# Performance work log

Hardware: AMD Instinct MI355X
Metric: run time of the kernel (lower is better)

Reference implementation:

```python
import jax, jax.numpy as jnp
import numpy as np

B, N, D = 256, 100000, 512
A, C, K = 256, 100, 32
EPS = 1e-8  # torch cosine_similarity eps


def setup_inputs() -> dict:
    key = jax.random.key(0)
    ks = jax.random.split(key, 10)
    s = lambda fan_in: 1.0 / np.sqrt(fan_in)
    return {
        "query_feat": jax.random.normal(ks[0], (B, D), jnp.float32),
        "memory_keys": jax.random.normal(ks[1], (N, D), jnp.float32),
        # query_dense: Linear(D, A)
        "Wq": jax.random.uniform(ks[2], (D, A), jnp.float32, -s(D), s(D)),
        "bq": jax.random.uniform(ks[3], (A,), jnp.float32, -s(D), s(D)),
        # memory_dense: Linear(D, A)
        "Wm": jax.random.uniform(ks[4], (D, A), jnp.float32, -s(D), s(D)),
        "bm": jax.random.uniform(ks[5], (A,), jnp.float32, -s(D), s(D)),
        # attention_score_dense: Linear(A, 1)
        "Ws": jax.random.uniform(ks[6], (A, 1), jnp.float32, -s(A), s(A)),
        "bs": jax.random.uniform(ks[7], (1,), jnp.float32, -s(A), s(A)),
        # classification_layer: Linear(2*D, C)
        "Wc": jax.random.uniform(ks[8], (2 * D, C), jnp.float32, -s(2 * D), s(2 * D)),
        "bc": jax.random.uniform(ks[9], (C,), jnp.float32, -s(2 * D), s(2 * D)),
    }


def reference(query_feat, memory_keys, Wq, bq, Wm, bm, Ws, bs, Wc, bc):
    # query embedding (visual encoder output) + relu
    q = jax.nn.relu(query_feat)  # [B, D]
    # ---- knn_search: cosine similarity + topk + gather ----
    qn = jnp.linalg.norm(q, axis=-1)            # [B]
    kn = jnp.linalg.norm(memory_keys, axis=-1)  # [N]
    sim = (q @ memory_keys.T) / jnp.maximum(qn[:, None] * kn[None, :], EPS)  # [B, N]
    _, idx = jax.lax.top_k(sim, K)              # [B, K]
    knn = memory_keys[idx]                      # [B, K, D]
    # ---- MemoryAttentionModule ----
    # tanh(query_dense(q)[:,None,:] + memory_dense(knn)) -> score -> softmax over K
    h = jnp.tanh((q @ Wq + bq)[:, None, :] + knn @ Wm + bm)  # [B, K, A]
    scores = h @ Ws + bs                                      # [B, K, 1]
    w = jax.nn.softmax(scores, axis=1)                        # [B, K, 1]
    attended = jnp.sum(w * knn, axis=1)                       # [B, D]
    # ---- classification ----
    merged = jnp.concatenate([q, attended], axis=1)           # [B, 2D]
    return merged @ Wc + bc                                   # [B, C]
```

## Files before the change

### kernel.cpp

```cpp
#include <hip/hip_runtime.h>
#include <hip/hip_bf16.h>
#include <hip/hip_fp16.h>

#define BQ    256
#define NKEY  100000
#define DD    512
#define AD    256
#define CD    100
#define KSEL  32
#define KB    64
#define NB    1563
#define CPQ   (NB*12)

#define NPART 8
#define WTOP  12
#define NC2   (NPART*4*WTOP)
#define TLA   6

typedef __attribute__((ext_vector_type(8))) short  short8_t;
typedef __attribute__((ext_vector_type(8))) __bf16 bf16x8;
typedef __attribute__((ext_vector_type(4))) float  f32x4;

__device__ __forceinline__ unsigned short f2bf(float x) {
  unsigned int u = __float_as_uint(x);
  return (unsigned short)((u + 0x7FFFu + ((u >> 16) & 1u)) >> 16);
}
__device__ __forceinline__ unsigned short f2bf_n(float x) {
  __bf16 h = (__bf16)x;
  return __builtin_bit_cast(unsigned short, h);
}
__device__ __forceinline__ float bf2f(unsigned short h) {
  return __uint_as_float(((unsigned int)h) << 16);
}
__device__ __forceinline__ f32x4 mfma_bf16(short8_t a, short8_t b, f32x4 c) {
  return __builtin_amdgcn_mfma_f32_16x16x32_bf16(
      __builtin_bit_cast(bf16x8, a), __builtin_bit_cast(bf16x8, b), c, 0, 0, 0);
}
__device__ __forceinline__ float fast_tanh(float x) {
  x = fminf(fmaxf(x, -15.f), 15.f);
  float e = __expf(2.f * x);
  return (e - 1.f) * __builtin_amdgcn_rcpf(e + 1.f);
}

template<int T>
__device__ __forceinline__ void topk_insert(float (&v)[T], int (&ix)[T], float val, int idx) {
  if (val <= v[T-1]) return;
  v[T-1] = val; ix[T-1] = idx;
  #pragma unroll
  for (int j = T-1; j > 0; --j) {
    bool sw = v[j] > v[j-1];
    float tv = sw ? v[j] : v[j-1];  float uv = sw ? v[j-1] : v[j];
    int   ti = sw ? ix[j] : ix[j-1]; int  ui = sw ? ix[j-1] : ix[j];
    v[j-1] = tv; v[j] = uv; ix[j-1] = ti; ix[j] = ui;
  }
}

__global__ __launch_bounds__(256) void k0_prep(const float* __restrict__ qfeat,
                                               const float* __restrict__ Wm,
                                               float* __restrict__ qr,
                                               unsigned short* __restrict__ qf,
                                               float* __restrict__ qn,
                                               unsigned short* __restrict__ wmf) {
  int b = blockIdx.x, t = threadIdx.x;
  if (b >= BQ) {
    int i = (b - BQ)*256 + t;
    int d = i >> 8, a = i & 255;
    wmf[(((a>>4)*64 + (d>>3))*16 + (a&15))*8 + (d&7)] = f2bf(Wm[i]);
    return;
  }
  float s = 0.f;
  #pragma unroll
  for (int p = 0; p < 2; ++p) {
    int k = t + p*256;
    float v = qfeat[b*DD + k];
    v = v > 0.f ? v : 0.f;
    qr[b*DD + k] = v;
    qf[(((b>>4)*64 + (k>>3))*16 + (b&15))*8 + (k&7)] = f2bf(v);
    s += v*v;
  }
  __shared__ float red[4];
  #pragma unroll
  for (int st = 1; st < 64; st <<= 1) s += __shfl_xor(s, st, 64);
  if ((t & 63) == 0) red[t>>6] = s;
  __syncthreads();
  if (t == 0) qn[b] = sqrtf(red[0]+red[1]+red[2]+red[3]);
}

__global__ __launch_bounds__(256) void k_qq(const float* __restrict__ Wq,
                                            const unsigned short* __restrict__ qf,
                                            const float* __restrict__ bq,
                                            const float* __restrict__ bm,
                                            float* __restrict__ qq) {
  __shared__ unsigned short wb[64*16*8];
  int bn = blockIdx.x & 15, rg = blockIdx.x >> 4;
  int t = threadIdx.x;
  int w = t >> 6, l = t & 63, g = l >> 4, c = l & 15;
  #pragma unroll
  for (int i = 0; i < 32; ++i) {
    int d = i*16 + (t>>4); int a = t & 15;
    wb[((d>>3)*16 + a)*8 + (d&7)] = f2bf(Wq[d*AD + bn*16 + a]);
  }
  __syncthreads();
  const short8_t* qf8 = (const short8_t*)qf;
  const short8_t* wb8 = (const short8_t*)wb;
  f32x4 acc = (f32x4){0.f,0.f,0.f,0.f};
  int M = rg*4 + w;
  for (int kt = 0; kt < 16; ++kt) {
    short8_t bfr = wb8[(kt*4 + g)*16 + c];
    short8_t afr = qf8[(M*64 + kt*4 + g)*16 + c];
    acc = mfma_bf16(afr, bfr, acc);
  }
  int col = bn*16 + c;
  float bias = bq[col] + bm[col];
  #pragma unroll
  for (int r = 0; r < 4; ++r)
    qq[(M*16 + g*4 + r)*AD + col] = acc[r] + bias;
}

__global__ __launch_bounds__(256) void k1_sim(const float* __restrict__ keys,
                                              const unsigned short* __restrict__ qf,
                                              unsigned int* __restrict__ cand) {
  __shared__ short8_t Abf8[64*8];
  __shared__ float invkn[64];

  int b = blockIdx.x, t = threadIdx.x;
  int kb0 = b*KB;
  int w = t >> 6, l = t & 63, g = l >> 4, c = l & 15;

  f32x4 acc[4][4];
  #pragma unroll
  for (int m = 0; m < 4; ++m)
    #pragma unroll
    for (int n = 0; n < 4; ++n) acc[m][n] = (f32x4){0.f,0.f,0.f,0.f};

  const short8_t* qf8 = (const short8_t*)qf;

  int r1 = t >> 3, gb = t & 7;
  int r2 = 32 + r1;
  int swz = gb ^ (r1 & 7);
  int row1 = kb0 + r1; row1 = row1 < NKEY ? row1 : NKEY-1;
  int row2 = kb0 + r2; row2 = row2 < NKEY ? row2 : NKEY-1;
  const float* src1 = keys + (size_t)row1*DD + gb*8;
  const float* src2 = keys + (size_t)row2*DD + gb*8;
  float ksq1 = 0.f, ksq2 = 0.f;

  short8_t Bcur[2][4];
  #pragma unroll
  for (int kt = 0; kt < 2; ++kt)
    #pragma unroll
    for (int n = 0; n < 4; ++n)
      Bcur[kt][n] = qf8[((w*4 + n)*64 + kt*4 + g)*16 + c];
  __builtin_amdgcn_sched_barrier(0);
  float4 Ge[4], Go[4];
  Ge[0] = *(const float4*)(src1);      Ge[1] = *(const float4*)(src1 + 4);
  Ge[2] = *(const float4*)(src2);      Ge[3] = *(const float4*)(src2 + 4);
  __builtin_amdgcn_sched_barrier(0);
  Go[0] = *(const float4*)(src1 + 64); Go[1] = *(const float4*)(src1 + 68);
  Go[2] = *(const float4*)(src2 + 64); Go[3] = *(const float4*)(src2 + 68);

  auto body = [&](int ks8, float4 (&Gc)[4]) {
    if (ks8 < 7) asm volatile("s_waitcnt vmcnt(4)" ::: "memory");
    else         asm volatile("s_waitcnt vmcnt(0)" ::: "memory");
    ksq1 += Gc[0].x*Gc[0].x + Gc[0].y*Gc[0].y + Gc[0].z*Gc[0].z + Gc[0].w*Gc[0].w
          + Gc[1].x*Gc[1].x + Gc[1].y*Gc[1].y + Gc[1].z*Gc[1].z + Gc[1].w*Gc[1].w;
    ksq2 += Gc[2].x*Gc[2].x + Gc[2].y*Gc[2].y + Gc[2].z*Gc[2].z + Gc[2].w*Gc[2].w
          + Gc[3].x*Gc[3].x + Gc[3].y*Gc[3].y + Gc[3].z*Gc[3].z + Gc[3].w*Gc[3].w;
    short8_t w1, w2;
    w1[0] = (short)f2bf_n(Gc[0].x); w1[1] = (short)f2bf_n(Gc[0].y);
    w1[2] = (short)f2bf_n(Gc[0].z); w1[3] = (short)f2bf_n(Gc[0].w);
    w1[4] = (short)f2bf_n(Gc[1].x); w1[5] = (short)f2bf_n(Gc[1].y);
    w1[6] = (short)f2bf_n(Gc[1].z); w1[7] = (short)f2bf_n(Gc[1].w);
    w2[0] = (short)f2bf_n(Gc[2].x); w2[1] = (short)f2bf_n(Gc[2].y);
    w2[2] = (short)f2bf_n(Gc[2].z); w2[3] = (short)f2bf_n(Gc[2].w);
    w2[4] = (short)f2bf_n(Gc[3].x); w2[5] = (short)f2bf_n(Gc[3].y);
    w2[6] = (short)f2bf_n(Gc[3].z); w2[7] = (short)f2bf_n(Gc[3].w);
    __builtin_amdgcn_s_barrier();
    Abf8[r1*8 + swz] = w1;
    Abf8[r2*8 + swz] = w2;
    short8_t Bnxt[2][4];
    if (ks8 < 7) {
      #pragma unroll
      for (int kt = 0; kt < 2; ++kt)
        #pragma unroll
        for (int n = 0; n < 4; ++n)
          Bnxt[kt][n] = qf8[((w*4 + n)*64 + (ks8+1)*8 + kt*4 + g)*16 + c];
    }
    __builtin_amdgcn_sched_barrier(0);
    if (ks8 < 6) {
      Gc[0] = *(const float4*)(src1 + (ks8+2)*64);
      Gc[1] = *(const float4*)(src1 + (ks8+2)*64 + 4);
      Gc[2] = *(const float4*)(src2 + (ks8+2)*64);
      Gc[3] = *(const float4*)(src2 + (ks8+2)*64 + 4);
    }
    asm volatile("s_waitcnt lgkmcnt(0)" ::: "memory");
    __builtin_amdgcn_s_barrier();
    __builtin_amdgcn_sched_barrier(0);
    int p = c & 7;
    #pragma unroll
    for (int kt = 0; kt < 2; ++kt) {
      #pragma unroll
      for (int m = 0; m < 4; ++m) {
        short8_t A = Abf8[(m*16 + c)*8 + ((kt*4 + g) ^ p)];
        #pragma unroll
        for (int n = 0; n < 4; ++n) acc[m][n] = mfma_bf16(A, Bcur[kt][n], acc[m][n]);
      }
    }
    if (ks8 < 7) {
      #pragma unroll
      for (int kt = 0; kt < 2; ++kt)
        #pragma unroll
        for (int n = 0; n < 4; ++n) Bcur[kt][n] = Bnxt[kt][n];
    }
  };

  #pragma unroll
  for (int ks8 = 0; ks8 < 8; ++ks8) {
    if (ks8 & 1) body(ks8, Go);
    else         body(ks8, Ge);
  }

  ksq1 += __shfl_xor(ksq1, 1, 64); ksq1 += __shfl_xor(ksq1, 2, 64); ksq1 += __shfl_xor(ksq1, 4, 64);
  ksq2 += __shfl_xor(ksq2, 1, 64); ksq2 += __shfl_xor(ksq2, 2, 64); ksq2 += __shfl_xor(ksq2, 4, 64);
  if ((t & 7) == 0) {
    invkn[r1] = ksq1 > 0.f ? rsqrtf(ksq1) : 0.f;
    invkn[r2] = ksq2 > 0.f ? rsqrtf(ksq2) : 0.f;
  }
  __syncthreads();

  float ikv[16];
  #pragma unroll
  for (int m = 0; m < 4; ++m)
    #pragma unroll
    for (int r = 0; r < 4; ++r) ikv[m*4 + r] = invkn[m*16 + g*4 + r];

  #pragma unroll
  for (int n = 0; n < 4; ++n) {
    float v1 = -3.0e38f, v2 = -3.0e38f, v3 = -3.0e38f;
    int   i1 = 0, i2 = 0, i3 = 0;
    #pragma unroll
    for (int m = 0; m < 4; ++m)
      #pragma unroll
      for (int r = 0; r < 4; ++r) {
        int lid = m*16 + g*4 + r;
        bool valid = (kb0 + lid) < NKEY;
        float v = valid ? acc[m][n][r] * ikv[m*4 + r] : -3.0e38f;
        bool gt1 = v > v1, gt2 = v > v2, gt3 = v > v3;
        v3 = gt2 ? v2 : (gt3 ? v : v3);  i3 = gt2 ? i2 : (gt3 ? lid : i3);
        v2 = gt1 ? v1 : (gt2 ? v : v2);  i2 = gt1 ? i1 : (gt2 ? lid : i2);
        v1 = gt1 ? v  : v1;              i1 = gt1 ? lid : i1;
      }
    int q = w*64 + n*16 + c;
    unsigned int base = ((unsigned int)q*NB + (unsigned int)b)*12u + (unsigned int)g*3u;
    cand[base + 0] = ((unsigned int)__half_as_ushort(__float2half(v1)) << 16) | (unsigned int)i1;
    cand[base + 1] = ((unsigned int)__half_as_ushort(__float2half(v2)) << 16) | (unsigned int)i2;
    cand[base + 2] = ((unsigned int)__half_as_ushort(__float2half(v3)) << 16) | (unsigned int)i3;
  }
}

__global__ __launch_bounds__(256) void k2a_reduce(const unsigned int* __restrict__ cand,
                                                  const float* __restrict__ qr,
                                                  const float* __restrict__ qn,
                                                  const float* __restrict__ keys,
                                                  float* __restrict__ wtopv,
                                                  int* __restrict__ wtopi) {
  int bid = blockIdx.x;
  int q = bid >> 3, p = bid & 7;
  int t = threadIdx.x, w = t >> 6, l = t & 63;
  const unsigned int* cq = cand + (size_t)q * CPQ;

  const int PER_PART = (CPQ + NPART - 1) / NPART;
  const int PER_WAVE = (PER_PART + 3) / 4;
  int pbase = p * PER_PART;
  int start = pbase + w * PER_WAVE;
  int end   = pbase + PER_PART;
  if (start + PER_WAVE < end) end = start + PER_WAVE;
  if (end > CPQ) end = CPQ;

  float v[TLA]; int ix[TLA];
  #pragma unroll
  for (int j = 0; j < TLA; ++j) { v[j] = -INFINITY; ix[j] = -1; }
  for (int i = start + l; i < end; i += 64) {
    unsigned int pk = cq[i];
    float val = __half2float(__ushort_as_half((unsigned short)(pk >> 16)));
    int bb = i / 12;
    int idx = (bb << 6) | (int)(pk & 63u);
    topk_insert<TLA>(v, ix, val, idx);
  }

  int idxs[WTOP];
  for (int it = 0; it < WTOP; ++it) {
    float bv = v[0]; int bx = ix[0]; int bl = l;
    #pragma unroll
    for (int sft = 1; sft < 64; sft <<= 1) {
      float ov = __shfl_xor(bv, sft, 64);
      int  oxx = __shfl_xor(bx, sft, 64);
      int  ol  = __shfl_xor(bl, sft, 64);
      bool take = (ov > bv) || (ov == bv && ol < bl);
      if (take) { bv = ov; bx = oxx; bl = ol; }
    }
    idxs[it] = bx;
    if (l == bl) {
      #pragma unroll
      for (int j = 0; j < TLA-1; ++j) { v[j] = v[j+1]; ix[j] = ix[j+1]; }
      v[TLA-1] = -INFINITY; ix[TLA-1] = -1;
    }
  }

  const float4* q4 = (const float4*)(qr + (size_t)q*DD + l*8);
  float4 qa0 = q4[0], qa1 = q4[1];
  float qnv = qn[q];
  int obase = (q * NPART + p) * 4 * WTOP + w * WTOP;

  int nidx = idxs[0];
  const float4* kr = (const float4*)(keys + (size_t)((nidx < 0 || nidx >= NKEY) ? 0 : nidx)*DD + l*8);
  float4 k0v = kr[0], k1v = kr[1];
  for (int j = 0; j < WTOP; ++j) {
    int curidx = idxs[j];
    bool bad = (curidx < 0) || (curidx >= NKEY);
    float4 c0 = k0v, c1 = k1v;
    if (j + 1 < WTOP) {
      nidx = idxs[j+1];
      kr = (const float4*)(keys + (size_t)((nidx < 0 || nidx >= NKEY) ? 0 : nidx)*DD + l*8);
      k0v = kr[0]; k1v = kr[1];
    }
    float dot = qa0.x*c0.x + qa0.y*c0.y + qa0.z*c0.z + qa0.w*c0.w
              + qa1.x*c1.x + qa1.y*c1.y + qa1.z*c1.z + qa1.w*c1.w;
    float ks  = c0.x*c0.x + c0.y*c0.y + c0.z*c0.z + c0.w*c0.w
              + c1.x*c1.x + c1.y*c1.y + c1.z*c1.z + c1.w*c1.w;
    #pragma unroll
    for (int sft = 1; sft < 64; sft <<= 1) {
      dot += __shfl_xor(dot, sft, 64);
      ks  += __shfl_xor(ks,  sft, 64);
    }
    if (l == 0) {
      float den = fmaxf(qnv * sqrtf(ks), 1e-8f);
      wtopv[obase + j] = bad ? -1e30f : dot/den;
      wtopi[obase + j] = bad ? 0 : curidx;
    }
  }
}

__global__ __launch_bounds__(256) void k23ab(const float* __restrict__ wtopv,
                                             const int* __restrict__ wtopi,
                                             const float* __restrict__ keys,
                                             const float* __restrict__ qq,
                                             const unsigned short* __restrict__ wmf,
                                             const float* __restrict__ Ws,
                                             const float* __restrict__ bsc,
                                             unsigned short* __restrict__ attf) {
  int q = blockIdx.x, t = threadIdx.x, w = t >> 6, l = t & 63, g = l >> 4, c = l & 15;
  __shared__ float simx[NC2];
  __shared__ int   sidx[NC2];
  __shared__ int   fl[KSEL];
  __shared__ float qqb[256];
  __shared__ float wsl[256];
  __shared__ unsigned short knnb[32*520];
  __shared__ float spart[4][32];
  __shared__ float wexp[32];

  qqb[t] = qq[q*AD + t];
  wsl[t] = Ws[t];
  for (int i = t; i < NC2; i += 256) {
    simx[i] = wtopv[q*NC2 + i];
    int idx = wtopi[q*NC2 + i];
    sidx[i] = (idx < 0 || idx >= NKEY) ? 0 : idx;
  }
  __syncthreads();

  if (w == 0) {
    float a[6]; int id[6];
    #pragma unroll
    for (int j = 0; j < 6; ++j) { a[j] = simx[j*64 + l]; id[j] = sidx[j*64 + l]; }
    for (int it = 0; it < KSEL; ++it) {
      float bv = a[0]; int bx = id[0]; int bslot = 0;
      #pragma unroll
      for (int j = 1; j < 6; ++j) {
        bool take = (a[j] > bv) || (a[j] == bv && id[j] < bx);
        bv = take ? a[j] : bv; bx = take ? id[j] : bx; bslot = take ? j : bslot;
      }
      int bl = l;
      #pragma unroll
      for (int sft = 1; sft < 64; sft <<= 1) {
        float ov = __shfl_xor(bv, sft, 64);
        int  oxx = __shfl_xor(bx, sft, 64);
        int  ol  = __shfl_xor(bl, sft, 64);
        bool take = (ov > bv) || (ov == bv && oxx < bx);
        if (take) { bv = ov; bx = oxx; bl = ol; }
      }
      if (l == 0) fl[it] = bx;
      if (l == bl) {
        #pragma unroll
        for (int j = 0; j < 6; ++j) if (j == bslot) a[j] = -INFINITY;
      }
    }
  }
  __syncthreads();

  #pragma unroll 4
  for (int rr = 0; rr < 32; rr += 2) {
    int r = rr + (t >> 7);
    int row = fl[r];
    int d4 = t & 127;
    float4 v = *(const float4*)(keys + (size_t)row*DD + d4*4);
    ushort4 h; h.x = f2bf_n(v.x); h.y = f2bf_n(v.y); h.z = f2bf_n(v.z); h.w = f2bf_n(v.w);
    *(ushort4*)&knnb[r*520 + d4*4] = h;
  }
  __syncthreads();

  f32x4 acc[2][4];
  #pragma unroll
  for (int m = 0; m < 2; ++m)
    #pragma unroll
    for (int n = 0; n < 4; ++n) acc[m][n] = (f32x4){0.f,0.f,0.f,0.f};
  const short8_t* wmf8 = (const short8_t*)wmf;
  for (int ks = 0; ks < 16; ++ks) {
    short8_t af[2], bf[4];
    #pragma unroll
    for (int m = 0; m < 2; ++m) af[m] = *(const short8_t*)&knnb[(m*16 + c)*520 + ks*32 + g*8];
    #pragma unroll
    for (int n = 0; n < 4; ++n) bf[n] = wmf8[((w*4 + n)*64 + ks*4 + g)*16 + c];
    #pragma unroll
    for (int m = 0; m < 2; ++m)
      #pragma unroll
      for (int n = 0; n < 4; ++n) acc[m][n] = mfma_bf16(af[m], bf[n], acc[m][n]);
  }

  float p[8] = {0.f,0.f,0.f,0.f,0.f,0.f,0.f,0.f};
  #pragma unroll
  for (int n = 0; n < 4; ++n) {
    int a = w*64 + n*16 + c;
    float qv = qqb[a], wv = wsl[a];
    #pragma unroll
    for (int m = 0; m < 2; ++m)
      #pragma unroll
      for (int r = 0; r < 4; ++r)
        p[m*4 + r] += fast_tanh(acc[m][n][r] + qv) * wv;
  }
  #pragma unroll
  for (int sft = 1; sft < 16; sft <<= 1)
    #pragma unroll
    for (int i = 0; i < 8; ++i) p[i] += __shfl_xor(p[i], sft, 64);
  if (c == 0) {
    #pragma unroll
    for (int m = 0; m < 2; ++m)
      #pragma unroll
      for (int r = 0; r < 4; ++r) spart[w][m*16 + g*4 + r] = p[m*4 + r];
  }
  __syncthreads();

  if (t < 32) {
    float s = spart[0][t] + spart[1][t] + spart[2][t] + spart[3][t] + bsc[0];
    float mx = s;
    #pragma unroll
    for (int sft = 1; sft < 32; sft <<= 1) mx = fmaxf(mx, __shfl_xor(mx, sft, 64));
    float e = __expf(s - mx);
    float su = e;
    #pragma unroll
    for (int sft = 1; sft < 32; sft <<= 1) su += __shfl_xor(su, sft, 64);
    wexp[t] = e / su;
  }
  __syncthreads();

  #pragma unroll
  for (int pth = 0; pth < 2; ++pth) {
    int d = t + pth*256;
    float s = 0.f;
    #pragma unroll
    for (int k = 0; k < 32; ++k) s += wexp[k] * bf2f(knnb[k*520 + d]);
    attf[(((q>>4)*64 + (d>>3))*16 + (q&15))*8 + (d&7)] = f2bf(s);
  }
}

__global__ __launch_bounds__(256) void k3b_cls(const float* __restrict__ Wc,
                                               const unsigned short* __restrict__ qf,
                                               const unsigned short* __restrict__ attf,
                                               const float* __restrict__ bc,
                                               float* __restrict__ out) {
  __shared__ unsigned short wb[128*16*8];
  int bn = blockIdx.x % 7, rg = blockIdx.x / 7;
  int t = threadIdx.x;
  int w = t >> 6, l = t & 63, g = l >> 4, c = l & 15;
  #pragma unroll
  for (int i = 0; i < 64; ++i) {
    int d = i*16 + (t>>4); int a = t & 15;
    int col = bn*16 + a;
    float vv = (col < CD) ? Wc[d*CD + col] : 0.f;
    wb[((d>>3)*16 + a)*8 + (d&7)] = f2bf(vv);
  }
  __syncthreads();
  const short8_t* qf8 = (const short8_t*)qf;
  const short8_t* af8 = (const short8_t*)attf;
  const short8_t* wb8 = (const short8_t*)wb;
  int M = rg*4 + w;
  f32x4 acc = (f32x4){0.f,0.f,0.f,0.f};
  for (int kt = 0; kt < 32; ++kt) {
    short8_t bfr = wb8[(kt*4 + g)*16 + c];
    const short8_t* asrc = (kt < 16) ? qf8 : af8;
    int kbase = (kt & 15)*4 + g;
    short8_t afr = asrc[(M*64 + kbase)*16 + c];
    acc = mfma_bf16(afr, bfr, acc);
  }
  int col = bn*16 + c;
  if (col < CD) {
    float bias = bc[col];
    #pragma unroll
    for (int r = 0; r < 4; ++r)
      out[(M*16 + g*4 + r)*CD + col] = acc[r] + bias;
  }
}

extern "C" void kernel_launch(void* const* d_in, const int* in_sizes, int n_in,
                              void* d_out, int out_size, void* d_ws, size_t ws_size,
                              hipStream_t stream) {
  const float* qfeat = (const float*)d_in[0];
  const float* keys  = (const float*)d_in[1];
  const float* Wq    = (const float*)d_in[2];
  const float* bq    = (const float*)d_in[3];
  const float* Wm    = (const float*)d_in[4];
  const float* bm    = (const float*)d_in[5];
  const float* Ws    = (const float*)d_in[6];
  const float* bsc   = (const float*)d_in[7];
  const float* Wc    = (const float*)d_in[8];
  const float* bc    = (const float*)d_in[9];
  float* out = (float*)d_out;

  char* ws = (char*)d_ws;
  unsigned short* qf   = (unsigned short*)(ws + 0);
  float*          qr   = (float*)(ws + 262144);
  float*          qn   = (float*)(ws + 786432);
  unsigned short* wmf  = (unsigned short*)(ws + 787456);
  float*          qq   = (float*)(ws + 1049600);
  unsigned short* attf = (unsigned short*)(ws + 1311744);
  float*          wtopv= (float*)(ws + 1573888);
  int*            wtopi= (int*)(ws + 1967104);
  unsigned int*   cand = (unsigned int*)(ws + 2360320);

  k0_prep   <<<768,      256, 0, stream>>>(qfeat, Wm, qr, qf, qn, wmf);
  k_qq      <<<64,       256, 0, stream>>>(Wq, qf, bq, bm, qq);
  k1_sim    <<<NB,       256, 0, stream>>>(keys, qf, cand);
  k2a_reduce<<<BQ*NPART, 256, 0, stream>>>(cand, qr, qn, keys, wtopv, wtopi);
  k23ab     <<<BQ,       256, 0, stream>>>(wtopv, wtopi, keys, qq, wmf, Ws, bsc, attf);
  k3b_cls   <<<28,       256, 0, stream>>>(Wc, qf, attf, bc, out);
}
```

Measured before the change: 173.7 us.

## Defer exact fp32 rescoring to a 64-candidate shortlist in the final selection kernel

The partial-reduce kernel now emits its per-wave top candidates with their approximate fp16 scores instead of fetching every key and recomputing exact cosine similarity for all 384 candidates per query. The attention kernel selects the 64 best approximate candidates, rescores only those in fp32 using the original keys and query norm, then picks the final top 32. This cuts the random key gathers per query from 384 to 64. The trade-off is a longer serial selection loop in one wave, and some accuracy risk if a true top-32 key falls outside the approximate top 64.

```diff
diff --git a/kernel.cpp b/kernel.cpp
--- a/kernel.cpp
+++ b/kernel.cpp
@@ -16,6 +16,7 @@
 #define WTOP  12
 #define NC2   (NPART*4*WTOP)
 #define TLA   6
+#define NRES  64
 
 typedef __attribute__((ext_vector_type(8))) short  short8_t;
 typedef __attribute__((ext_vector_type(8))) __bf16 bf16x8;
@@ -258,9 +259,6 @@
 }
 
 __global__ __launch_bounds__(256) void k2a_reduce(const unsigned int* __restrict__ cand,
-                                                  const float* __restrict__ qr,
-                                                  const float* __restrict__ qn,
-                                                  const float* __restrict__ keys,
                                                   float* __restrict__ wtopv,
                                                   int* __restrict__ wtopi) {
   int bid = blockIdx.x;
@@ -287,7 +285,7 @@
     topk_insert<TLA>(v, ix, val, idx);
   }
 
-  int idxs[WTOP];
+  int obase = (q * NPART + p) * 4 * WTOP + w * WTOP;
   for (int it = 0; it < WTOP; ++it) {
     float bv = v[0]; int bx = ix[0]; int bl = l;
     #pragma unroll
@@ -298,50 +296,19 @@
       bool take = (ov > bv) || (ov == bv && ol < bl);
       if (take) { bv = ov; bx = oxx; bl = ol; }
     }
-    idxs[it] = bx;
+    if (l == 0) { wtopv[obase + it] = bv; wtopi[obase + it] = bx; }
     if (l == bl) {
       #pragma unroll
       for (int j = 0; j < TLA-1; ++j) { v[j] = v[j+1]; ix[j] = ix[j+1]; }
       v[TLA-1] = -INFINITY; ix[TLA-1] = -1;
     }
   }
-
-  const float4* q4 = (const float4*)(qr + (size_t)q*DD + l*8);
-  float4 qa0 = q4[0], qa1 = q4[1];
-  float qnv = qn[q];
-  int obase = (q * NPART + p) * 4 * WTOP + w * WTOP;
-
-  int nidx = idxs[0];
-  const float4* kr = (const float4*)(keys + (size_t)((nidx < 0 || nidx >= NKEY) ? 0 : nidx)*DD + l*8);
-  float4 k0v = kr[0], k1v = kr[1];
-  for (int j = 0; j < WTOP; ++j) {
-    int curidx = idxs[j];
-    bool bad = (curidx < 0) || (curidx >= NKEY);
-    float4 c0 = k0v, c1 = k1v;
-    if (j + 1 < WTOP) {
-      nidx = idxs[j+1];
-      kr = (const float4*)(keys + (size_t)((nidx < 0 || nidx >= NKEY) ? 0 : nidx)*DD + l*8);
-      k0v = kr[0]; k1v = kr[1];
-    }
-    float dot = qa0.x*c0.x + qa0.y*c0.y + qa0.z*c0.z + qa0.w*c0.w
-              + qa1.x*c1.x + qa1.y*c1.y + qa1.z*c1.z + qa1.w*c1.w;
-    float ks  = c0.x*c0.x + c0.y*c0.y + c0.z*c0.z + c0.w*c0.w
-              + c1.x*c1.x + c1.y*c1.y + c1.z*c1.z + c1.w*c1.w;
-    #pragma unroll
-    for (int sft = 1; sft < 64; sft <<= 1) {
-      dot += __shfl_xor(dot, sft, 64);
-      ks  += __shfl_xor(ks,  sft, 64);
-    }
-    if (l == 0) {
-      float den = fmaxf(qnv * sqrtf(ks), 1e-8f);
-      wtopv[obase + j] = bad ? -1e30f : dot/den;
-      wtopi[obase + j] = bad ? 0 : curidx;
-    }
-  }
 }
 
 __global__ __launch_bounds__(256) void k23ab(const float* __restrict__ wtopv,
                                              const int* __restrict__ wtopi,
+                                             const float* __restrict__ qr,
+                                             const float* __restrict__ qn,
                                              const float* __restrict__ keys,
                                              const float* __restrict__ qq,
                                              const unsigned short* __restrict__ wmf,
@@ -351,6 +318,9 @@
   int q = blockIdx.x, t = threadIdx.x, w = t >> 6, l = t & 63, g = l >> 4, c = l & 15;
   __shared__ float simx[NC2];
   __shared__ int   sidx[NC2];
+  __shared__ int   c64[NRES];
+  __shared__ float exv[NRES];
+  __shared__ int   exi[NRES];
   __shared__ int   fl[KSEL];
   __shared__ float qqb[256];
   __shared__ float wsl[256];
@@ -362,8 +332,7 @@
   wsl[t] = Ws[t];
   for (int i = t; i < NC2; i += 256) {
     simx[i] = wtopv[q*NC2 + i];
-    int idx = wtopi[q*NC2 + i];
-    sidx[i] = (idx < 0 || idx >= NKEY) ? 0 : idx;
+    sidx[i] = wtopi[q*NC2 + i];
   }
   __syncthreads();
 
@@ -371,7 +340,7 @@
     float a[6]; int id[6];
     #pragma unroll
     for (int j = 0; j < 6; ++j) { a[j] = simx[j*64 + l]; id[j] = sidx[j*64 + l]; }
-    for (int it = 0; it < KSEL; ++it) {
+    for (int it = 0; it < NRES; ++it) {
       float bv = a[0]; int bx = id[0]; int bslot = 0;
       #pragma unroll
       for (int j = 1; j < 6; ++j) {
@@ -387,11 +356,63 @@
         bool take = (ov > bv) || (ov == bv && oxx < bx);
         if (take) { bv = ov; bx = oxx; bl = ol; }
       }
-      if (l == 0) fl[it] = bx;
+      if (l == 0) c64[it] = bx;
       if (l == bl) {
         #pragma unroll
         for (int j = 0; j < 6; ++j) if (j == bslot) a[j] = -INFINITY;
       }
+    }
+  }
+  __syncthreads();
+
+  {
+    const float4* q4 = (const float4*)(qr + (size_t)q*DD + l*8);
+    float4 qa0 = q4[0], qa1 = q4[1];
+    float qnv = qn[q];
+    int idx = c64[w*16];
+    const float4* kr = (const float4*)(keys + (size_t)((idx < 0 || idx >= NKEY) ? 0 : idx)*DD + l*8);
+    float4 k0v = kr[0], k1v = kr[1];
+    for (int j = 0; j < 16; ++j) {
+      int curidx = idx;
+      bool bad = (curidx < 0) || (curidx >= NKEY);
+      float4 c0 = k0v, c1 = k1v;
+      if (j + 1 < 16) {
+        idx = c64[w*16 + j + 1];
+        kr = (const float4*)(keys + (size_t)((idx < 0 || idx >= NKEY) ? 0 : idx)*DD + l*8);
+        k0v = kr[0]; k1v = kr[1];
+      }
+      float dot = qa0.x*c0.x + qa0.y*c0.y + qa0.z*c0.z + qa0.w*c0.w
+                + qa1.x*c1.x + qa1.y*c1.y + qa1.z*c1.z + qa1.w*c1.w;
+      float ks  = c0.x*c0.x + c0.y*c0.y + c0.z*c0.z + c0.w*c0.w
+                + c1.x*c1.x + c1.y*c1.y + c1.z*c1.z + c1.w*c1.w;
+      #pragma unroll
+      for (int sft = 1; sft < 64; sft <<= 1) {
+        dot += __shfl_xor(dot, sft, 64);
+        ks  += __shfl_xor(ks,  sft, 64);
+      }
+      if (l == 0) {
+        float den = fmaxf(qnv * sqrtf(ks), 1e-8f);
+        exv[w*16 + j] = bad ? -1e30f : dot/den;
+        exi[w*16 + j] = bad ? 0 : curidx;
+      }
+    }
+  }
+  __syncthreads();
+
+  if (w == 0) {
+    float a0 = exv[l]; int i0 = exi[l];
+    for (int it = 0; it < KSEL; ++it) {
+      float bv = a0; int bx = i0; int bl = l;
+      #pragma unroll
+      for (int sft = 1; sft < 64; sft <<= 1) {
+        float ov = __shfl_xor(bv, sft, 64);
+        int  oxx = __shfl_xor(bx, sft, 64);
+        int  ol  = __shfl_xor(bl, sft, 64);
+        bool take = (ov > bv) || (ov == bv && oxx < bx);
+        if (take) { bv = ov; bx = oxx; bl = ol; }
+      }
+      if (l == 0) fl[it] = bx;
+      if (l == bl) a0 = -INFINITY;
     }
   }
   __syncthreads();
@@ -538,7 +559,7 @@
   k0_prep   <<<768,      256, 0, stream>>>(qfeat, Wm, qr, qf, qn, wmf);
   k_qq      <<<64,       256, 0, stream>>>(Wq, qf, bq, bm, qq);
   k1_sim    <<<NB,       256, 0, stream>>>(keys, qf, cand);
-  k2a_reduce<<<BQ*NPART, 256, 0, stream>>>(cand, qr, qn, keys, wtopv, wtopi);
-  k23ab     <<<BQ,       256, 0, stream>>>(wtopv, wtopi, keys, qq, wmf, Ws, bsc, attf);
+  k2a_reduce<<<BQ*NPART, 256, 0, stream>>>(cand, wtopv, wtopi);
+  k23ab     <<<BQ,       256, 0, stream>>>(wtopv, wtopi, qr, qn, keys, qq, wmf, Ws, bsc, attf);
   k3b_cls   <<<28,       256, 0, stream>>>(Wc, qf, attf, bc, out);
 }
```

Measured after the change: 208.0 us. +19.7%, slower.
